# Kernel optimization log

Hardware: AMD Instinct MI355X
Metric: run time of the kernel (lower is better)

Reference implementation:

```python
import jax, jax.numpy as jnp
import numpy as np

B, L, D, H, SPD = 16, 512, 768, 12, 5
DH = D // H
LN_EPS = 1e-5
CLAMP_MIN = 1e-6


def setup_inputs() -> dict:
    key = jax.random.key(0)
    ks = jax.random.split(key, 8)
    s = 1.0 / np.sqrt(D)
    return {
        "tgt": jax.random.normal(ks[0], (B, L, D), jnp.float32),
        "query_pos": jax.random.normal(ks[1], (B, L, D), jnp.float32),
        "pairwise_locs": jax.random.normal(ks[2], (B, L, L, SPD), jnp.float32),
        "Wq": jax.random.normal(ks[3], (D, D), jnp.float32) * s,
        "bq": jnp.zeros((D,), jnp.float32),
        "Wk": jax.random.normal(ks[4], (D, D), jnp.float32) * s,
        "bk": jnp.zeros((D,), jnp.float32),
        "Wv": jax.random.normal(ks[5], (D, D), jnp.float32) * s,
        "bv": jnp.zeros((D,), jnp.float32),
        "Wo": jax.random.normal(ks[6], (D, D), jnp.float32) * s,
        "bo": jnp.zeros((D,), jnp.float32),
        "Wloc": jax.random.normal(ks[7], (SPD, H), jnp.float32) * (1.0 / np.sqrt(SPD)),
        "bloc": jnp.zeros((H,), jnp.float32),
        "ln_g": jnp.ones((D,), jnp.float32),
        "ln_b": jnp.zeros((D,), jnp.float32),
    }


def _layer_norm(x, g, b):
    mu = jnp.mean(x, axis=-1, keepdims=True)
    var = jnp.mean(jnp.square(x - mu), axis=-1, keepdims=True)
    return g * (x - mu) * jax.lax.rsqrt(var + LN_EPS) + b


def reference(tgt, query_pos, pairwise_locs, Wq, bq, Wk, bk, Wv, bv, Wo, bo, Wloc, bloc, ln_g, ln_b):
    # forward_post path: q = k = tgt + query_pos; v = tgt
    qk_in = tgt + query_pos
    q = (qk_in @ Wq + bq).reshape(B, L, H, DH)   # [B,L,H,DH]
    k = (qk_in @ Wk + bk).reshape(B, L, H, DH)
    v = (tgt @ Wv + bv).reshape(B, L, H, DH)

    scale = np.float32(1.0 / np.sqrt(DH))
    attn = jnp.einsum('blhd,bthd->bhlt', q, k) * scale   # [B,H,L,L]

    # spatial fusion 'mul': relu(Linear(pairwise_locs)) -> log-domain additive bias
    loc_attn = jax.nn.relu(pairwise_locs @ Wloc + bloc)   # [B,L,L,H]
    loc_attn = jnp.transpose(loc_attn, (0, 3, 1, 2))      # [B,H,L,L]
    fused = jax.nn.softmax(jnp.log(jnp.clip(loc_attn, CLAMP_MIN, None)) + attn, axis=-1)

    out = jnp.einsum('bhlt,bthd->blhd', fused, v).reshape(B, L, D)
    out = out @ Wo + bo                                   # attn output (tgt2)

    # residual + (dropout p=0) + LayerNorm
    return _layer_norm(tgt + out, ln_g, ln_b)
```

## Files before the change

kernel.cpp:

```cpp
#include <hip/hip_runtime.h>
#include <math.h>

#define BB 16
#define LL 512
#define DD 768
#define HH 12
#define DHH 64
#define SPDD 5
#define MM (BB*LL)
#define LN_EPS 1e-5f
#define CLAMP_MINV 1e-6f

typedef __attribute__((ext_vector_type(8))) short bf8_t;
typedef __attribute__((ext_vector_type(4))) float f4_t;

__device__ __forceinline__ short f2bf(float x) {
    unsigned u = __builtin_bit_cast(unsigned, x);
    unsigned r = (u + 0x7FFFu + ((u >> 16) & 1u)) >> 16;
    return (short)r;
}

__device__ __forceinline__ void gld16(const short* g, short* l) {
    __builtin_amdgcn_global_load_lds(
        (const __attribute__((address_space(1))) unsigned int*)g,
        (__attribute__((address_space(3))) unsigned int*)l,
        16, 0, 0);
}

__device__ __forceinline__ float block_sum(float v, float* red, int tid) {
    #pragma unroll
    for (int off = 32; off; off >>= 1) v += __shfl_down(v, off, 64);
    __syncthreads();
    if ((tid & 63) == 0) red[tid >> 6] = v;
    __syncthreads();
    return red[0] + red[1] + red[2] + red[3];
}

__global__ __launch_bounds__(256) void wtrans_kernel(
    const float* __restrict__ W0, const float* __restrict__ W1,
    const float* __restrict__ W2, const float* __restrict__ W3,
    short* __restrict__ O0, short* __restrict__ O1,
    short* __restrict__ O2, short* __restrict__ O3)
{
    const float* W; short* O;
    switch (blockIdx.z) {
        case 0: W = W0; O = O0; break;
        case 1: W = W1; O = O1; break;
        case 2: W = W2; O = O2; break;
        default: W = W3; O = O3; break;
    }
    __shared__ float T[64][65];
    const int n0 = blockIdx.x * 64, k0 = blockIdx.y * 64;
    const int tid = threadIdx.x;
    {
        const int kk = tid >> 4, nv = (tid & 15) * 4;
        #pragma unroll
        for (int i = 0; i < 4; ++i) {
            const int k = kk + i * 16;
            const float4 v = *(const float4*)(W + (size_t)(k0 + k) * DD + n0 + nv);
            T[k][nv + 0] = v.x; T[k][nv + 1] = v.y;
            T[k][nv + 2] = v.z; T[k][nv + 3] = v.w;
        }
    }
    __syncthreads();
    {
        const int n = tid >> 2, kc = (tid & 3) * 16;
        short tmp[16];
        #pragma unroll
        for (int i = 0; i < 16; ++i) tmp[i] = f2bf(T[kc + i][n]);
        short* dst = O + (size_t)(n0 + n) * DD + k0 + kc;
        *(bf8_t*)dst       = *(bf8_t*)tmp;
        *(bf8_t*)(dst + 8) = *(bf8_t*)(tmp + 8);
    }
}

__global__ __launch_bounds__(256) void cast_inputs(
    const float* __restrict__ tgt, const float* __restrict__ qpos,
    short* __restrict__ aqk, short* __restrict__ av)
{
    const size_t base = ((size_t)blockIdx.x * 256 + threadIdx.x) * 8;
    const float4 t0 = *(const float4*)(tgt + base);
    const float4 t1 = *(const float4*)(tgt + base + 4);
    const float4 p0 = *(const float4*)(qpos + base);
    const float4 p1 = *(const float4*)(qpos + base + 4);
    short v[8], q[8];
    v[0] = f2bf(t0.x); v[1] = f2bf(t0.y); v[2] = f2bf(t0.z); v[3] = f2bf(t0.w);
    v[4] = f2bf(t1.x); v[5] = f2bf(t1.y); v[6] = f2bf(t1.z); v[7] = f2bf(t1.w);
    q[0] = f2bf(t0.x + p0.x); q[1] = f2bf(t0.y + p0.y);
    q[2] = f2bf(t0.z + p0.z); q[3] = f2bf(t0.w + p0.w);
    q[4] = f2bf(t1.x + p1.x); q[5] = f2bf(t1.y + p1.y);
    q[6] = f2bf(t1.z + p1.z); q[7] = f2bf(t1.w + p1.w);
    *(bf8_t*)(av + base)  = *(bf8_t*)v;
    *(bf8_t*)(aqk + base) = *(bf8_t*)q;
}

template<int MODE, bool FUSE>
__global__ __launch_bounds__(256) void gemm_mfma(
    const short* __restrict__ A,
    const short* __restrict__ Wa, const float* __restrict__ ba, void* __restrict__ oa,
    const short* __restrict__ Wb, const float* __restrict__ bb, void* __restrict__ ob)
{
    __shared__ short As[128 * 64];
    __shared__ short Bs[128 * 64];
    int bx = blockIdx.x;
    const int by = blockIdx.y;
    const short* Wt; const float* bias; void* out;
    if (FUSE && bx >= 6) { Wt = Wb; bias = bb; out = ob; bx -= 6; }
    else                 { Wt = Wa; bias = ba; out = oa; }
    const int n0 = bx * 128, m0 = by * 128;
    const int tid = threadIdx.x;
    const int w = tid >> 6, lane = tid & 63;
    const int quad = lane >> 4, l16 = lane & 15;
    const int wm = w & 1, wn = w >> 1;

    const int sr = w * 8 + (lane >> 3);
    const int sp = lane & 7;

    f4_t acc[4][4];
    #pragma unroll
    for (int i = 0; i < 4; ++i)
        #pragma unroll
        for (int j = 0; j < 4; ++j) acc[i][j] = (f4_t){0.f, 0.f, 0.f, 0.f};

    for (int k0 = 0; k0 < DD; k0 += 64) {
        __syncthreads();
        #pragma unroll
        for (int ra = 0; ra < 4; ++ra) {
            const int r = sr + ra * 32;
            const int c = sp ^ (r & 7);
            const int ldso = ra * 2048 + w * 512 + lane * 8;
            gld16(A  + (size_t)(m0 + r) * DD + k0 + c * 8, As + ldso);
            gld16(Wt + (size_t)(n0 + r) * DD + k0 + c * 8, Bs + ldso);
        }
        __syncthreads();
        #pragma unroll
        for (int s = 0; s < 2; ++s) {
            bf8_t a[4], b[4];
            #pragma unroll
            for (int i = 0; i < 4; ++i) {
                const int rA = wm * 64 + i * 16 + l16;
                const int pA = (s * 4 + quad) ^ (rA & 7);
                a[i] = *(const bf8_t*)(As + rA * 64 + pA * 8);
                const int rB = wn * 64 + i * 16 + l16;
                const int pB = (s * 4 + quad) ^ (rB & 7);
                b[i] = *(const bf8_t*)(Bs + rB * 64 + pB * 8);
            }
            #pragma unroll
            for (int i = 0; i < 4; ++i)
                #pragma unroll
                for (int j = 0; j < 4; ++j)
                    acc[i][j] = __builtin_amdgcn_mfma_f32_16x16x32_bf16(a[i], b[j], acc[i][j], 0, 0, 0);
        }
    }

    float bv[4];
    #pragma unroll
    for (int j = 0; j < 4; ++j) bv[j] = bias[n0 + wn * 64 + j * 16 + l16];
    #pragma unroll
    for (int i = 0; i < 4; ++i) {
        #pragma unroll
        for (int j = 0; j < 4; ++j) {
            const int n = n0 + wn * 64 + j * 16 + l16;
            #pragma unroll
            for (int r = 0; r < 4; ++r) {
                const int m = m0 + wm * 64 + i * 16 + quad * 4 + r;
                const float val = acc[i][j][r] + bv[j];
                if (MODE == 0) {
                    ((float*)out)[(size_t)m * DD + n] = val;
                } else {
                    const int b_ = m >> 9, l = m & 511;
                    const int h = n >> 6, d = n & 63;
                    if (MODE == 1)
                        ((short*)out)[(((size_t)(b_ * HH + h)) * LL + l) * DHH + d] = f2bf(val);
                    else
                        ((short*)out)[(((size_t)(b_ * HH + h)) * DHH + d) * LL + l] = f2bf(val);
                }
            }
        }
    }
}

__global__ __launch_bounds__(256) void attn_mfma(
    const short* __restrict__ Q, const short* __restrict__ K,
    const short* __restrict__ Vt, const float* __restrict__ ploc,
    const float* __restrict__ Wloc, const float* __restrict__ bloc,
    short* __restrict__ out)
{
    __shared__ short Ks[64 * 64];
    __shared__ short Vs[64 * 64];
    __shared__ float bs[64 * 65];
    __shared__ short Ps[4][16 * 64];

    const int qt = blockIdx.x, h = blockIdx.y, b = blockIdx.z;
    const int tid = threadIdx.x;
    const int w = tid >> 6, lane = tid & 63;
    const int quad = lane >> 4, l16 = lane & 15;
    const int q0 = qt * 64;
    const size_t bh = (size_t)b * HH + h;

    float wl[SPDD];
    #pragma unroll
    for (int s = 0; s < SPDD; ++s) wl[s] = Wloc[s * HH + h];
    const float blc = bloc[h];

    const int qr = q0 + w * 16 + l16;
    const bf8_t aq0 = *(const bf8_t*)(Q + (bh * LL + qr) * DHH + quad * 8);
    const bf8_t aq1 = *(const bf8_t*)(Q + (bh * LL + qr) * DHH + quad * 8 + 32);

    f4_t o[4];
    #pragma unroll
    for (int dj = 0; dj < 4; ++dj) o[dj] = (f4_t){0.f, 0.f, 0.f, 0.f};
    float m_row[4], l_row[4];
    #pragma unroll
    for (int r = 0; r < 4; ++r) { m_row[r] = -1e30f; l_row[r] = 0.f; }

    const short* Kg = K  + bh * LL * DHH;
    const short* Vg = Vt + bh * DHH * LL;

    for (int t0 = 0; t0 < LL; t0 += 64) {
        __syncthreads();
        {
            const short* src = Kg + t0 * DHH + tid * 16;
            *(bf8_t*)(Ks + tid * 16)     = *(const bf8_t*)(src);
            *(bf8_t*)(Ks + tid * 16 + 8) = *(const bf8_t*)(src + 8);
        }
        {
            const int d = tid >> 2, ch = (tid & 3) * 16;
            const short* src = Vg + (size_t)d * LL + t0 + ch;
            *(bf8_t*)(Vs + d * 64 + ch)     = *(const bf8_t*)(src);
            *(bf8_t*)(Vs + d * 64 + ch + 8) = *(const bf8_t*)(src + 8);
        }
        {
            const int l = tid >> 2, ts = (tid & 3) * 16;
            const float* pp = ploc + (((size_t)b * LL + q0 + l) * LL + t0 + ts) * SPDD;
            #pragma unroll
            for (int i = 0; i < 16; ++i) {
                float la = blc;
                #pragma unroll
                for (int s = 0; s < SPDD; ++s) la += pp[i * SPDD + s] * wl[s];
                la = fmaxf(fmaxf(la, 0.f), CLAMP_MINV);
                bs[l * 65 + ts + i] = __logf(la);
            }
        }
        __syncthreads();

        f4_t sv[4];
        #pragma unroll
        for (int j = 0; j < 4; ++j) {
            const bf8_t b0 = *(const bf8_t*)(Ks + (j * 16 + l16) * 64 + quad * 8);
            const bf8_t b1 = *(const bf8_t*)(Ks + (j * 16 + l16) * 64 + quad * 8 + 32);
            f4_t c = (f4_t){0.f, 0.f, 0.f, 0.f};
            c = __builtin_amdgcn_mfma_f32_16x16x32_bf16(aq0, b0, c, 0, 0, 0);
            c = __builtin_amdgcn_mfma_f32_16x16x32_bf16(aq1, b1, c, 0, 0, 0);
            sv[j] = c;
        }
        #pragma unroll
        for (int j = 0; j < 4; ++j)
            #pragma unroll
            for (int r = 0; r < 4; ++r) {
                const int lrel = w * 16 + quad * 4 + r;
                sv[j][r] = sv[j][r] * 0.125f + bs[lrel * 65 + j * 16 + l16];
            }
        #pragma unroll
        for (int r = 0; r < 4; ++r) {
            float mx = fmaxf(fmaxf(sv[0][r], sv[1][r]), fmaxf(sv[2][r], sv[3][r]));
            mx = fmaxf(mx, __shfl_xor(mx, 1, 16));
            mx = fmaxf(mx, __shfl_xor(mx, 2, 16));
            mx = fmaxf(mx, __shfl_xor(mx, 4, 16));
            mx = fmaxf(mx, __shfl_xor(mx, 8, 16));
            const float mn = fmaxf(m_row[r], mx);
            const float al = __expf(m_row[r] - mn);
            m_row[r] = mn;
            float rs = 0.f;
            #pragma unroll
            for (int j = 0; j < 4; ++j) {
                const float p = __expf(sv[j][r] - mn);
                sv[j][r] = p;
                rs += p;
            }
            rs += __shfl_xor(rs, 1, 16);
            rs += __shfl_xor(rs, 2, 16);
            rs += __shfl_xor(rs, 4, 16);
            rs += __shfl_xor(rs, 8, 16);
            l_row[r] = l_row[r] * al + rs;
            #pragma unroll
            for (int dj = 0; dj < 4; ++dj) o[dj][r] *= al;
        }
        short* Pw = Ps[w];
        #pragma unroll
        for (int r = 0; r < 4; ++r)
            #pragma unroll
            for (int j = 0; j < 4; ++j)
                Pw[(quad * 4 + r) * 64 + j * 16 + l16] = f2bf(sv[j][r]);

        const bf8_t ap0 = *(const bf8_t*)(Pw + l16 * 64 + quad * 8);
        const bf8_t ap1 = *(const bf8_t*)(Pw + l16 * 64 + quad * 8 + 32);
        #pragma unroll
        for (int dj = 0; dj < 4; ++dj) {
            const bf8_t b0 = *(const bf8_t*)(Vs + (dj * 16 + l16) * 64 + quad * 8);
            const bf8_t b1 = *(const bf8_t*)(Vs + (dj * 16 + l16) * 64 + quad * 8 + 32);
            o[dj] = __builtin_amdgcn_mfma_f32_16x16x32_bf16(ap0, b0, o[dj], 0, 0, 0);
            o[dj] = __builtin_amdgcn_mfma_f32_16x16x32_bf16(ap1, b1, o[dj], 0, 0, 0);
        }
    }

    #pragma unroll
    for (int r = 0; r < 4; ++r) {
        const int l = q0 + w * 16 + quad * 4 + r;
        const float inv = 1.f / l_row[r];
        short* op = out + ((size_t)b * LL + l) * DD + h * DHH;
        #pragma unroll
        for (int dj = 0; dj < 4; ++dj)
            op[dj * 16 + l16] = f2bf(o[dj][r] * inv);
    }
}

__global__ __launch_bounds__(256) void ln_kernel(
    const float* __restrict__ x, const float* __restrict__ tgt,
    const float* __restrict__ g, const float* __restrict__ bta,
    float* __restrict__ out)
{
    const int row = blockIdx.x;
    const int tid = threadIdx.x;
    __shared__ float red[4];

    const float* xp = x + (size_t)row * DD;
    const float* tp = tgt + (size_t)row * DD;

    float vals[3];
    float s = 0.f;
    #pragma unroll
    for (int i = 0; i < 3; ++i) {
        const float v = xp[tid + i * 256] + tp[tid + i * 256];
        vals[i] = v;
        s += v;
    }
    s = block_sum(s, red, tid);
    const float mu = s * (1.f / 768.f);

    float vs = 0.f;
    #pragma unroll
    for (int i = 0; i < 3; ++i) {
        const float dv = vals[i] - mu;
        vs += dv * dv;
    }
    vs = block_sum(vs, red, tid);
    const float rstd = rsqrtf(vs * (1.f / 768.f) + LN_EPS);

    #pragma unroll
    for (int i = 0; i < 3; ++i) {
        const int cidx = tid + i * 256;
        out[(size_t)row * DD + cidx] = g[cidx] * (vals[i] - mu) * rstd + bta[cidx];
    }
}

extern "C" void kernel_launch(void* const* d_in, const int* in_sizes, int n_in,
                              void* d_out, int out_size, void* d_ws, size_t ws_size,
                              hipStream_t stream) {
    const float* tgt   = (const float*)d_in[0];
    const float* qpos  = (const float*)d_in[1];
    const float* ploc  = (const float*)d_in[2];
    const float* Wq    = (const float*)d_in[3];
    const float* bq    = (const float*)d_in[4];
    const float* Wk    = (const float*)d_in[5];
    const float* bk    = (const float*)d_in[6];
    const float* Wv    = (const float*)d_in[7];
    const float* bv    = (const float*)d_in[8];
    const float* Wo    = (const float*)d_in[9];
    const float* bo    = (const float*)d_in[10];
    const float* Wloc  = (const float*)d_in[11];
    const float* bloc  = (const float*)d_in[12];
    const float* ln_g  = (const float*)d_in[13];
    const float* ln_b  = (const float*)d_in[14];

    const size_t NQ = (size_t)MM * DD;
    const size_t NW = (size_t)DD * DD;
    short* qb   = (short*)d_ws;
    short* kb   = qb  + NQ;
    short* vtb  = kb  + NQ;
    short* aob  = vtb + NQ;
    short* aqk  = aob + NQ;
    short* av   = aqk + NQ;
    float* pbuf = (float*)aqk;
    short* wqt  = av + NQ;
    short* wkt  = wqt + NW;
    short* wvt  = wkt + NW;
    short* wot  = wvt + NW;

    wtrans_kernel<<<dim3(12, 12, 4), 256, 0, stream>>>(Wq, Wk, Wv, Wo, wqt, wkt, wvt, wot);
    cast_inputs<<<3072, 256, 0, stream>>>(tgt, qpos, aqk, av);

    gemm_mfma<1, true ><<<dim3(12, 64), 256, 0, stream>>>(aqk, wqt, bq, qb, wkt, bk, kb);
    gemm_mfma<2, false><<<dim3(6, 64),  256, 0, stream>>>(av,  wvt, bv, vtb, nullptr, nullptr, nullptr);

    attn_mfma<<<dim3(8, 12, 16), 256, 0, stream>>>(qb, kb, vtb, ploc, Wloc, bloc, aob);

    gemm_mfma<0, false><<<dim3(6, 64),  256, 0, stream>>>(aob, wot, bo, pbuf, nullptr, nullptr, nullptr);

    ln_kernel<<<MM, 256, 0, stream>>>(pbuf, tgt, ln_g, ln_b, (float*)d_out);
}
```

Measured before the change: 411.0 us.

## Precompute bf16 log spatial bias, merge QKV GEMMs, swizzle attention LDS tiles

Adds a separate kernel that reads pairwise_locs once per (b,l,t) and writes the log-relu bias for all 12 heads as a bf16 [B,H,L,L] tensor. Before, each of the 12 head blocks re-read the fp32 5-wide locs tensor with strided loads. The attention kernel now loads this bias tile as short4 into a padded bf16 LDS buffer. The Q/K/V projections are merged into one launch, and the K, V and P tiles in LDS use XOR swizzles to avoid bank conflicts. In exchange it writes and reads a large extra bias buffer (about 100MB), rounds the bias to bf16, and only takes the precomputed path when the workspace is large enough.

```diff
diff --git a/kernel.cpp b/kernel.cpp
--- a/kernel.cpp
+++ b/kernel.cpp
@@ -18,6 +18,10 @@
     unsigned u = __builtin_bit_cast(unsigned, x);
     unsigned r = (u + 0x7FFFu + ((u >> 16) & 1u)) >> 16;
     return (short)r;
+}
+__device__ __forceinline__ float bf2f(short s) {
+    unsigned u = ((unsigned)(unsigned short)s) << 16;
+    return __builtin_bit_cast(float, u);
 }
 
 __device__ __forceinline__ void gld16(const short* g, short* l) {
@@ -94,19 +98,57 @@
     *(bf8_t*)(aqk + base) = *(bf8_t*)q;
 }
 
-template<int MODE, bool FUSE>
-__global__ __launch_bounds__(256) void gemm_mfma(
-    const short* __restrict__ A,
-    const short* __restrict__ Wa, const float* __restrict__ ba, void* __restrict__ oa,
-    const short* __restrict__ Wb, const float* __restrict__ bb, void* __restrict__ ob)
+__global__ __launch_bounds__(256) void bias_kernel(
+    const float* __restrict__ ploc, const float* __restrict__ Wloc,
+    const float* __restrict__ bloc, short* __restrict__ out)
+{
+    const int g   = blockIdx.x * 256 + threadIdx.x;
+    const int tch = g & 63;
+    const int l   = (g >> 6) & 511;
+    const int b   = g >> 15;
+    const int t0  = tch * 8;
+
+    float p[40];
+    const float* src = ploc + (((size_t)b * LL + l) * LL + t0) * SPDD;
+    #pragma unroll
+    for (int i = 0; i < 10; ++i)
+        *(float4*)(p + i * 4) = *(const float4*)(src + i * 4);
+
+    #pragma unroll
+    for (int h = 0; h < HH; ++h) {
+        float wl[SPDD];
+        #pragma unroll
+        for (int s = 0; s < SPDD; ++s) wl[s] = Wloc[s * HH + h];
+        const float bl = bloc[h];
+        short o[8];
+        #pragma unroll
+        for (int i = 0; i < 8; ++i) {
+            float la = bl;
+            #pragma unroll
+            for (int s = 0; s < SPDD; ++s) la += p[i * SPDD + s] * wl[s];
+            la = fmaxf(fmaxf(la, 0.f), CLAMP_MINV);
+            o[i] = f2bf(__logf(la));
+        }
+        *(bf8_t*)(out + (((size_t)(b * HH + h) * LL + l) * LL + t0)) = *(bf8_t*)o;
+    }
+}
+
+__global__ __launch_bounds__(256) void gemm_qkv(
+    const short* __restrict__ Aqk, const short* __restrict__ Av,
+    const short* __restrict__ Wq, const float* __restrict__ bq, short* __restrict__ oq,
+    const short* __restrict__ Wk, const float* __restrict__ bk, short* __restrict__ ok,
+    const short* __restrict__ Wv, const float* __restrict__ bv, short* __restrict__ ov)
 {
     __shared__ short As[128 * 64];
     __shared__ short Bs[128 * 64];
-    int bx = blockIdx.x;
+    const int seg = blockIdx.x / 6;
+    const int bx = blockIdx.x % 6;
     const int by = blockIdx.y;
-    const short* Wt; const float* bias; void* out;
-    if (FUSE && bx >= 6) { Wt = Wb; bias = bb; out = ob; bx -= 6; }
-    else                 { Wt = Wa; bias = ba; out = oa; }
+    const short* A  = (seg == 2) ? Av : Aqk;
+    const short* Wt = (seg == 0) ? Wq : (seg == 1) ? Wk : Wv;
+    const float* bias = (seg == 0) ? bq : (seg == 1) ? bk : bv;
+    short* out = (seg == 0) ? oq : (seg == 1) ? ok : ov;
+
     const int n0 = bx * 128, m0 = by * 128;
     const int tid = threadIdx.x;
     const int w = tid >> 6, lane = tid & 63;
@@ -153,9 +195,9 @@
         }
     }
 
-    float bv[4];
-    #pragma unroll
-    for (int j = 0; j < 4; ++j) bv[j] = bias[n0 + wn * 64 + j * 16 + l16];
+    float bvv[4];
+    #pragma unroll
+    for (int j = 0; j < 4; ++j) bvv[j] = bias[n0 + wn * 64 + j * 16 + l16];
     #pragma unroll
     for (int i = 0; i < 4; ++i) {
         #pragma unroll
@@ -164,31 +206,96 @@
             #pragma unroll
             for (int r = 0; r < 4; ++r) {
                 const int m = m0 + wm * 64 + i * 16 + quad * 4 + r;
-                const float val = acc[i][j][r] + bv[j];
-                if (MODE == 0) {
-                    ((float*)out)[(size_t)m * DD + n] = val;
-                } else {
-                    const int b_ = m >> 9, l = m & 511;
-                    const int h = n >> 6, d = n & 63;
-                    if (MODE == 1)
-                        ((short*)out)[(((size_t)(b_ * HH + h)) * LL + l) * DHH + d] = f2bf(val);
-                    else
-                        ((short*)out)[(((size_t)(b_ * HH + h)) * DHH + d) * LL + l] = f2bf(val);
-                }
-            }
-        }
-    }
-}
-
+                const float val = acc[i][j][r] + bvv[j];
+                const int b_ = m >> 9, l = m & 511;
+                const int h = n >> 6, d = n & 63;
+                if (seg < 2)
+                    out[(((size_t)(b_ * HH + h)) * LL + l) * DHH + d] = f2bf(val);
+                else
+                    out[(((size_t)(b_ * HH + h)) * DHH + d) * LL + l] = f2bf(val);
+            }
+        }
+    }
+}
+
+__global__ __launch_bounds__(256) void gemm_o(
+    const short* __restrict__ A, const short* __restrict__ Wt,
+    const float* __restrict__ bias, float* __restrict__ out)
+{
+    __shared__ short As[128 * 64];
+    __shared__ short Bs[128 * 64];
+    const int bx = blockIdx.x, by = blockIdx.y;
+    const int n0 = bx * 128, m0 = by * 128;
+    const int tid = threadIdx.x;
+    const int w = tid >> 6, lane = tid & 63;
+    const int quad = lane >> 4, l16 = lane & 15;
+    const int wm = w & 1, wn = w >> 1;
+    const int sr = w * 8 + (lane >> 3);
+    const int sp = lane & 7;
+
+    f4_t acc[4][4];
+    #pragma unroll
+    for (int i = 0; i < 4; ++i)
+        #pragma unroll
+        for (int j = 0; j < 4; ++j) acc[i][j] = (f4_t){0.f, 0.f, 0.f, 0.f};
+
+    for (int k0 = 0; k0 < DD; k0 += 64) {
+        __syncthreads();
+        #pragma unroll
+        for (int ra = 0; ra < 4; ++ra) {
+            const int r = sr + ra * 32;
+            const int c = sp ^ (r & 7);
+            const int ldso = ra * 2048 + w * 512 + lane * 8;
+            gld16(A  + (size_t)(m0 + r) * DD + k0 + c * 8, As + ldso);
+            gld16(Wt + (size_t)(n0 + r) * DD + k0 + c * 8, Bs + ldso);
+        }
+        __syncthreads();
+        #pragma unroll
+        for (int s = 0; s < 2; ++s) {
+            bf8_t a[4], b[4];
+            #pragma unroll
+            for (int i = 0; i < 4; ++i) {
+                const int rA = wm * 64 + i * 16 + l16;
+                const int pA = (s * 4 + quad) ^ (rA & 7);
+                a[i] = *(const bf8_t*)(As + rA * 64 + pA * 8);
+                const int rB = wn * 64 + i * 16 + l16;
+                const int pB = (s * 4 + quad) ^ (rB & 7);
+                b[i] = *(const bf8_t*)(Bs + rB * 64 + pB * 8);
+            }
+            #pragma unroll
+            for (int i = 0; i < 4; ++i)
+                #pragma unroll
+                for (int j = 0; j < 4; ++j)
+                    acc[i][j] = __builtin_amdgcn_mfma_f32_16x16x32_bf16(a[i], b[j], acc[i][j], 0, 0, 0);
+        }
+    }
+
+    float bvv[4];
+    #pragma unroll
+    for (int j = 0; j < 4; ++j) bvv[j] = bias[n0 + wn * 64 + j * 16 + l16];
+    #pragma unroll
+    for (int i = 0; i < 4; ++i)
+        #pragma unroll
+        for (int j = 0; j < 4; ++j) {
+            const int n = n0 + wn * 64 + j * 16 + l16;
+            #pragma unroll
+            for (int r = 0; r < 4; ++r) {
+                const int m = m0 + wm * 64 + i * 16 + quad * 4 + r;
+                out[(size_t)m * DD + n] = acc[i][j][r] + bvv[j];
+            }
+        }
+}
+
+template<bool PRE>
 __global__ __launch_bounds__(256) void attn_mfma(
     const short* __restrict__ Q, const short* __restrict__ K,
-    const short* __restrict__ Vt, const float* __restrict__ ploc,
-    const float* __restrict__ Wloc, const float* __restrict__ bloc,
-    short* __restrict__ out)
+    const short* __restrict__ Vt, const short* __restrict__ LB,
+    const float* __restrict__ ploc, const float* __restrict__ Wloc,
+    const float* __restrict__ bloc, short* __restrict__ out)
 {
     __shared__ short Ks[64 * 64];
     __shared__ short Vs[64 * 64];
-    __shared__ float bs[64 * 65];
+    __shared__ short bs16[64 * 68];
     __shared__ short Ps[4][16 * 64];
 
     const int qt = blockIdx.x, h = blockIdx.y, b = blockIdx.z;
@@ -199,9 +306,12 @@
     const size_t bh = (size_t)b * HH + h;
 
     float wl[SPDD];
-    #pragma unroll
-    for (int s = 0; s < SPDD; ++s) wl[s] = Wloc[s * HH + h];
-    const float blc = bloc[h];
+    float blc = 0.f;
+    if (!PRE) {
+        #pragma unroll
+        for (int s = 0; s < SPDD; ++s) wl[s] = Wloc[s * HH + h];
+        blc = bloc[h];
+    }
 
     const int qr = q0 + w * 16 + l16;
     const bf8_t aq0 = *(const bf8_t*)(Q + (bh * LL + qr) * DHH + quad * 8);
@@ -216,30 +326,41 @@
 
     const short* Kg = K  + bh * LL * DHH;
     const short* Vg = Vt + bh * DHH * LL;
+    const short* Bg = PRE ? (LB + (bh * LL + q0) * LL) : nullptr;
+
+    const int srow = tid >> 2;
+    const int cb   = (tid & 3) * 2;
+    const int sw   = srow & 7;
 
     for (int t0 = 0; t0 < LL; t0 += 64) {
         __syncthreads();
         {
-            const short* src = Kg + t0 * DHH + tid * 16;
-            *(bf8_t*)(Ks + tid * 16)     = *(const bf8_t*)(src);
-            *(bf8_t*)(Ks + tid * 16 + 8) = *(const bf8_t*)(src + 8);
+            const short* src = Kg + (size_t)(t0 + srow) * DHH + cb * 8;
+            *(bf8_t*)(Ks + srow * 64 + ((cb ^ sw) * 8))       = *(const bf8_t*)(src);
+            *(bf8_t*)(Ks + srow * 64 + (((cb + 1) ^ sw) * 8)) = *(const bf8_t*)(src + 8);
         }
         {
-            const int d = tid >> 2, ch = (tid & 3) * 16;
-            const short* src = Vg + (size_t)d * LL + t0 + ch;
-            *(bf8_t*)(Vs + d * 64 + ch)     = *(const bf8_t*)(src);
-            *(bf8_t*)(Vs + d * 64 + ch + 8) = *(const bf8_t*)(src + 8);
+            const short* src = Vg + (size_t)srow * LL + t0 + cb * 8;
+            *(bf8_t*)(Vs + srow * 64 + ((cb ^ sw) * 8))       = *(const bf8_t*)(src);
+            *(bf8_t*)(Vs + srow * 64 + (((cb + 1) ^ sw) * 8)) = *(const bf8_t*)(src + 8);
         }
         {
             const int l = tid >> 2, ts = (tid & 3) * 16;
-            const float* pp = ploc + (((size_t)b * LL + q0 + l) * LL + t0 + ts) * SPDD;
-            #pragma unroll
-            for (int i = 0; i < 16; ++i) {
-                float la = blc;
+            if (PRE) {
+                const short* src = Bg + (size_t)l * LL + t0 + ts;
                 #pragma unroll
-                for (int s = 0; s < SPDD; ++s) la += pp[i * SPDD + s] * wl[s];
-                la = fmaxf(fmaxf(la, 0.f), CLAMP_MINV);
-                bs[l * 65 + ts + i] = __logf(la);
+                for (int i = 0; i < 4; ++i)
+                    *(short4*)(bs16 + l * 68 + ts + i * 4) = *(const short4*)(src + i * 4);
+            } else {
+                const float* pp = ploc + (((size_t)b * LL + q0 + l) * LL + t0 + ts) * SPDD;
+                #pragma unroll
+                for (int i = 0; i < 16; ++i) {
+                    float la = blc;
+                    #pragma unroll
+                    for (int s = 0; s < SPDD; ++s) la += pp[i * SPDD + s] * wl[s];
+                    la = fmaxf(fmaxf(la, 0.f), CLAMP_MINV);
+                    bs16[l * 68 + ts + i] = f2bf(__logf(la));
+                }
             }
         }
         __syncthreads();
@@ -247,8 +368,10 @@
         f4_t sv[4];
         #pragma unroll
         for (int j = 0; j < 4; ++j) {
-            const bf8_t b0 = *(const bf8_t*)(Ks + (j * 16 + l16) * 64 + quad * 8);
-            const bf8_t b1 = *(const bf8_t*)(Ks + (j * 16 + l16) * 64 + quad * 8 + 32);
+            const int rB = j * 16 + l16;
+            const int x = rB & 7;
+            const bf8_t b0 = *(const bf8_t*)(Ks + rB * 64 + ((quad ^ x) * 8));
+            const bf8_t b1 = *(const bf8_t*)(Ks + rB * 64 + (((quad + 4) ^ x) * 8));
             f4_t c = (f4_t){0.f, 0.f, 0.f, 0.f};
             c = __builtin_amdgcn_mfma_f32_16x16x32_bf16(aq0, b0, c, 0, 0, 0);
             c = __builtin_amdgcn_mfma_f32_16x16x32_bf16(aq1, b1, c, 0, 0, 0);
@@ -259,7 +382,7 @@
             #pragma unroll
             for (int r = 0; r < 4; ++r) {
                 const int lrel = w * 16 + quad * 4 + r;
-                sv[j][r] = sv[j][r] * 0.125f + bs[lrel * 65 + j * 16 + l16];
+                sv[j][r] = sv[j][r] * 0.125f + bf2f(bs16[lrel * 68 + j * 16 + l16]);
             }
         #pragma unroll
         for (int r = 0; r < 4; ++r) {
@@ -288,17 +411,23 @@
         }
         short* Pw = Ps[w];
         #pragma unroll
-        for (int r = 0; r < 4; ++r)
-            #pragma unroll
-            for (int j = 0; j < 4; ++j)
-                Pw[(quad * 4 + r) * 64 + j * 16 + l16] = f2bf(sv[j][r]);
-
-        const bf8_t ap0 = *(const bf8_t*)(Pw + l16 * 64 + quad * 8);
-        const bf8_t ap1 = *(const bf8_t*)(Pw + l16 * 64 + quad * 8 + 32);
+        for (int r = 0; r < 4; ++r) {
+            const int rp = quad * 4 + r, rp7 = rp & 7;
+            #pragma unroll
+            for (int j = 0; j < 4; ++j) {
+                const int t = j * 16 + l16;
+                Pw[rp * 64 + (((t >> 3) ^ rp7) * 8) + (t & 7)] = f2bf(sv[j][r]);
+            }
+        }
+        const int m7 = l16 & 7;
+        const bf8_t ap0 = *(const bf8_t*)(Pw + l16 * 64 + ((quad ^ m7) * 8));
+        const bf8_t ap1 = *(const bf8_t*)(Pw + l16 * 64 + (((quad + 4) ^ m7) * 8));
         #pragma unroll
         for (int dj = 0; dj < 4; ++dj) {
-            const bf8_t b0 = *(const bf8_t*)(Vs + (dj * 16 + l16) * 64 + quad * 8);
-            const bf8_t b1 = *(const bf8_t*)(Vs + (dj * 16 + l16) * 64 + quad * 8 + 32);
+            const int rB = dj * 16 + l16;
+            const int x = rB & 7;
+            const bf8_t b0 = *(const bf8_t*)(Vs + rB * 64 + ((quad ^ x) * 8));
+            const bf8_t b1 = *(const bf8_t*)(Vs + rB * 64 + (((quad + 4) ^ x) * 8));
             o[dj] = __builtin_amdgcn_mfma_f32_16x16x32_bf16(ap0, b0, o[dj], 0, 0, 0);
             o[dj] = __builtin_amdgcn_mfma_f32_16x16x32_bf16(ap1, b1, o[dj], 0, 0, 0);
         }
@@ -375,6 +504,8 @@
 
     const size_t NQ = (size_t)MM * DD;
     const size_t NW = (size_t)DD * DD;
+    const size_t NB = (size_t)BB * HH * LL * LL;
+
     short* qb   = (short*)d_ws;
     short* kb   = qb  + NQ;
     short* vtb  = kb  + NQ;
@@ -386,16 +517,25 @@
     short* wkt  = wqt + NW;
     short* wvt  = wkt + NW;
     short* wot  = wvt + NW;
+    short* lb   = wot + NW;
+
+    const size_t needed = (size_t)(6 * NQ + 4 * NW + NB) * 2;
+    const bool pre = (ws_size >= needed);
 
     wtrans_kernel<<<dim3(12, 12, 4), 256, 0, stream>>>(Wq, Wk, Wv, Wo, wqt, wkt, wvt, wot);
     cast_inputs<<<3072, 256, 0, stream>>>(tgt, qpos, aqk, av);
-
-    gemm_mfma<1, true ><<<dim3(12, 64), 256, 0, stream>>>(aqk, wqt, bq, qb, wkt, bk, kb);
-    gemm_mfma<2, false><<<dim3(6, 64),  256, 0, stream>>>(av,  wvt, bv, vtb, nullptr, nullptr, nullptr);
-
-    attn_mfma<<<dim3(8, 12, 16), 256, 0, stream>>>(qb, kb, vtb, ploc, Wloc, bloc, aob);
-
-    gemm_mfma<0, false><<<dim3(6, 64),  256, 0, stream>>>(aob, wot, bo, pbuf, nullptr, nullptr, nullptr);
+    if (pre)
+        bias_kernel<<<2048, 256, 0, stream>>>(ploc, Wloc, bloc, lb);
+
+    gemm_qkv<<<dim3(18, 64), 256, 0, stream>>>(aqk, av, wqt, bq, qb,
+                                               wkt, bk, kb, wvt, bv, vtb);
+
+    if (pre)
+        attn_mfma<true ><<<dim3(8, 12, 16), 256, 0, stream>>>(qb, kb, vtb, lb, ploc, Wloc, bloc, aob);
+    else
+        attn_mfma<false><<<dim3(8, 12, 16), 256, 0, stream>>>(qb, kb, vtb, nullptr, ploc, Wloc, bloc, aob);
+
+    gemm_o<<<dim3(6, 64), 256, 0, stream>>>(aob, wot, bo, pbuf);
 
     ln_kernel<<<MM, 256, 0, stream>>>(pbuf, tgt, ln_g, ln_b, (float*)d_out);
 }
```

New measurement: 400.9 us. 1.03x faster.
